# Performance work log

Hardware: AMD Instinct MI355X
Metric: run time of the kernel (lower is better)

## Reference

```python
import jax, jax.numpy as jnp
import numpy as np

D_MODEL = 1024
N_HEADS = 16
HEAD_DIM = D_MODEL // N_HEADS
D_FF = 4 * D_MODEL
LN_EPS = 1e-5


def setup_inputs() -> dict:
    key = jax.random.key(0)
    ks = jax.random.split(key, 12)
    B, T = 16, 512
    s = lambda fan_in: 1.0 / np.sqrt(fan_in)
    inp = {
        'x': jax.random.normal(ks[0], (B, T, D_MODEL), jnp.float32),
        # torch Linear layout: [out_features, in_features]
        'w_qkv': jax.random.normal(ks[1], (3 * D_MODEL, D_MODEL), jnp.float32) * s(D_MODEL),
        'w_proj': jax.random.normal(ks[2], (D_MODEL, D_MODEL), jnp.float32) * s(D_MODEL),
        'w_ff1': jax.random.normal(ks[3], (D_FF, D_MODEL), jnp.float32) * s(D_MODEL),
        'b_ff1': jax.random.normal(ks[4], (D_FF,), jnp.float32) * 0.02,
        'w_ff2': jax.random.normal(ks[5], (D_MODEL, D_FF), jnp.float32) * s(D_FF),
        'b_ff2': jax.random.normal(ks[6], (D_MODEL,), jnp.float32) * 0.02,
        'ln1_g': jnp.ones((D_MODEL,), jnp.float32),
        'ln1_b': jnp.zeros((D_MODEL,), jnp.float32),
        'ln2_g': jnp.ones((D_MODEL,), jnp.float32),
        'ln2_b': jnp.zeros((D_MODEL,), jnp.float32),
    }
    return inp


def _layernorm(x, g, b):
    mu = jnp.mean(x, axis=-1, keepdims=True)
    var = jnp.var(x, axis=-1, keepdims=True)
    return (x - mu) * jax.lax.rsqrt(var + LN_EPS) * g + b


def _block(x, w_qkv, w_proj, w_ff1, b_ff1, w_ff2, b_ff2, ln1_g, ln1_b, ln2_g, ln2_b):
    B, T, _ = x.shape
    a = _layernorm(x, ln1_g, ln1_b)
    qkv = a @ w_qkv.T  # [B,T,3D]
    q, k, v = jnp.split(qkv, 3, axis=-1)
    # [B,H,T,hd]
    rs = lambda t: t.reshape(B, T, N_HEADS, HEAD_DIM).transpose(0, 2, 1, 3)
    q, k, v = rs(q), rs(k), rs(v)
    scale = HEAD_DIM ** -0.5
    att = jnp.einsum('bhqd,bhkd->bhqk', q, k) * scale
    causal = jnp.tril(jnp.ones((T, T), bool))
    att = jnp.where(causal, att, jnp.float32(-10000.0))
    att = jax.nn.softmax(att, axis=-1)
    out = jnp.einsum('bhqk,bhkd->bhqd', att, v)
    out = out.transpose(0, 2, 1, 3).reshape(B, T, D_MODEL)
    x = x + out @ w_proj.T
    f = _layernorm(x, ln2_g, ln2_b)
    f = jax.nn.gelu(f @ w_ff1.T + b_ff1, approximate=False) @ w_ff2.T + b_ff2
    return x + f


def reference(x, w_qkv, w_proj, w_ff1, b_ff1, w_ff2, b_ff2, ln1_g, ln1_b, ln2_g, ln2_b):
    return _block(x, w_qkv, w_proj, w_ff1, b_ff1, w_ff2, b_ff2, ln1_g, ln1_b, ln2_g, ln2_b)
```

## Files before the change

kernel.cpp:

```cpp
#include <hip/hip_runtime.h>
#include <stdint.h>

typedef __bf16 bf16x8_t __attribute__((ext_vector_type(8)));
typedef float f32x4_t __attribute__((ext_vector_type(4)));
typedef unsigned short ushort8_t __attribute__((ext_vector_type(8)));

#define DEV __device__ __forceinline__

DEV unsigned short f2bf(float f) {
  union { float f; uint32_t u; } v; v.f = f;
  uint32_t r = v.u + 0x7FFFu + ((v.u >> 16) & 1u);
  return (unsigned short)(r >> 16);
}

DEV void gl_lds16(const void* g, void* l) {
  __builtin_amdgcn_global_load_lds(
      (const __attribute__((address_space(1))) void*)g,
      (__attribute__((address_space(3))) void*)l, 16, 0, 0);
}

DEV float gelu_f(float x) {
  const float y = x * 0.7071067811865475f;
  const float ay = fabsf(y);
  const float t = __builtin_amdgcn_rcpf(1.0f + 0.3275911f * ay);
  float p = fmaf(t, 1.061405429f, -1.453152027f);
  p = fmaf(t, p, 1.421413741f);
  p = fmaf(t, p, -0.284496736f);
  p = fmaf(t, p, 0.254829592f);
  p *= t;
  const float e = __expf(-ay * ay);
  float erfv = 1.0f - p * e;
  erfv = copysignf(erfv, y);
  return 0.5f * x * (1.0f + erfv);
}

__global__ __launch_bounds__(256) void cvt_all(const float* __restrict__ w0, unsigned short* __restrict__ o0,
                                               const float* __restrict__ w1, unsigned short* __restrict__ o1,
                                               const float* __restrict__ w2, unsigned short* __restrict__ o2,
                                               const float* __restrict__ w3, unsigned short* __restrict__ o3) {
  int i = blockIdx.x * 256 + threadIdx.x;
  const float* in; unsigned short* outp;
  if (i < 786432) { in = w0; outp = o0; }
  else if (i < 1048576) { in = w1; outp = o1; i -= 786432; }
  else if (i < 2097152) { in = w2; outp = o2; i -= 1048576; }
  else { in = w3; outp = o3; i -= 2097152; }
  float4 v = ((const float4*)in)[i];
  ushort4 o;
  o.x = f2bf(v.x); o.y = f2bf(v.y); o.z = f2bf(v.z); o.w = f2bf(v.w);
  ((ushort4*)outp)[i] = o;
}

__global__ __launch_bounds__(256) void ln_kernel(const float* __restrict__ x,
                                                 const float* __restrict__ g,
                                                 const float* __restrict__ b,
                                                 unsigned short* __restrict__ outp) {
  const int row = blockIdx.x * 4 + (threadIdx.x >> 6);
  const int lane = threadIdx.x & 63;
  const float4* xr = (const float4*)(x + (size_t)row * 1024);
  float4 v[4];
  float s = 0.f, s2 = 0.f;
#pragma unroll
  for (int j = 0; j < 4; ++j) {
    v[j] = xr[j * 64 + lane];
    s += v[j].x + v[j].y + v[j].z + v[j].w;
    s2 += v[j].x * v[j].x + v[j].y * v[j].y + v[j].z * v[j].z + v[j].w * v[j].w;
  }
#pragma unroll
  for (int off = 1; off < 64; off <<= 1) {
    s += __shfl_xor(s, off, 64);
    s2 += __shfl_xor(s2, off, 64);
  }
  const float mu = s * (1.0f / 1024.0f);
  const float var = s2 * (1.0f / 1024.0f) - mu * mu;
  const float rstd = rsqrtf(var + 1e-5f);
  ushort4* orow = (ushort4*)(outp + (size_t)row * 1024);
  const float4* gp = (const float4*)g;
  const float4* bp = (const float4*)b;
#pragma unroll
  for (int j = 0; j < 4; ++j) {
    float4 gv = gp[j * 64 + lane], bv = bp[j * 64 + lane];
    ushort4 o;
    o.x = f2bf((v[j].x - mu) * rstd * gv.x + bv.x);
    o.y = f2bf((v[j].y - mu) * rstd * gv.y + bv.y);
    o.z = f2bf((v[j].z - mu) * rstd * gv.z + bv.z);
    o.w = f2bf((v[j].w - mu) * rstd * gv.w + bv.w);
    orow[j * 64 + lane] = o;
  }
}

template <int MODE, int BM>
__global__ __launch_bounds__(256) void gemm_bt(const unsigned short* __restrict__ A,
                                               const unsigned short* __restrict__ B,
                                               float* __restrict__ Cf,
                                               unsigned short* __restrict__ Cb,
                                               const float* __restrict__ bias,
                                               const float* __restrict__ res,
                                               unsigned short* __restrict__ Vt,
                                               int M, int N, int K) {
  constexpr int MI = BM / 32;
  constexpr int RT = 8192 / BM;
  constexpr int ABUF = BM * 32;
  __shared__ unsigned short sA[2][ABUF];
  __shared__ unsigned short sB[2][128 * 32];
  const int tid = threadIdx.x;
  const int w = tid >> 6, lane = tid & 63;
  const int kg = lane >> 4, l16 = lane & 15;
  const int wm = (w & 1) * (BM / 2), wn = (w >> 1) * 64;

  const int cid = blockIdx.y * gridDim.x + blockIdx.x;
  const int colBase = (cid / RT) * 128;
  const int rowBase = (cid % RT) * BM;

  const int sr = (BM == 128) ? (tid >> 2) : ((tid >> 2) & 63);
  const int gc = ((tid & 3) ^ ((sr >> 1) & 3)) * 8;
  const unsigned short* gA = A + (size_t)(rowBase + sr) * K + gc;
  const unsigned short* gB = B + (size_t)(colBase + sr) * K + gc;

  f32x4_t acc[MI][4];
#pragma unroll
  for (int mi = 0; mi < MI; ++mi)
#pragma unroll
    for (int ni = 0; ni < 4; ++ni) acc[mi][ni] = (f32x4_t)0.0f;

  int offA[MI], offB[4];
  const int pc = (kg ^ ((l16 >> 1) & 3)) * 8;
#pragma unroll
  for (int i = 0; i < MI; ++i) offA[i] = (wm + i * 16 + l16) * 32 + pc;
#pragma unroll
  for (int i = 0; i < 4; ++i) offB[i] = (wn + i * 16 + l16) * 32 + pc;

  gl_lds16(gA, &sA[0][tid * 8]);
  if (BM == 128) gl_lds16(gA + (size_t)64 * K, &sA[0][2048 + tid * 8]);
  gl_lds16(gB, &sB[0][tid * 8]);
  gl_lds16(gB + (size_t)64 * K, &sB[0][2048 + tid * 8]);
  gA += 32; gB += 32;

  const int nk = K >> 5;
  for (int kt = 0; kt < nk; ++kt) {
    __syncthreads();
    if (kt + 1 < nk) {
      const int nb = (kt + 1) & 1;
      gl_lds16(gA, &sA[nb][tid * 8]);
      if (BM == 128) gl_lds16(gA + (size_t)64 * K, &sA[nb][2048 + tid * 8]);
      gl_lds16(gB, &sB[nb][tid * 8]);
      gl_lds16(gB + (size_t)64 * K, &sB[nb][2048 + tid * 8]);
      gA += 32; gB += 32;
    }
    const int par = kt & 1;
    bf16x8_t a[MI], b[4];
#pragma unroll
    for (int i = 0; i < MI; ++i) a[i] = *(const bf16x8_t*)(&sA[par][0] + offA[i]);
#pragma unroll
    for (int i = 0; i < 4; ++i) b[i] = *(const bf16x8_t*)(&sB[par][0] + offB[i]);
#pragma unroll
    for (int mi = 0; mi < MI; ++mi)
#pragma unroll
      for (int ni = 0; ni < 4; ++ni)
        acc[mi][ni] = __builtin_amdgcn_mfma_f32_16x16x32_bf16(a[mi], b[ni], acc[mi][ni], 0, 0, 0);
  }

#pragma unroll
  for (int mi = 0; mi < MI; ++mi) {
#pragma unroll
    for (int ni = 0; ni < 4; ++ni) {
      const int col = colBase + wn + ni * 16 + l16;
      if (MODE == 0 && colBase >= 2048) {
        const int c2 = col - 2048;
        const int hh = c2 >> 6, dd = c2 & 63;
        const int rw = rowBase + wm + mi * 16 + kg * 4;
        ushort4 pk;
        pk.x = f2bf(acc[mi][ni][0]);
        pk.y = f2bf(acc[mi][ni][1]);
        pk.z = f2bf(acc[mi][ni][2]);
        pk.w = f2bf(acc[mi][ni][3]);
        *(ushort4*)(Vt + (((size_t)(rw >> 9) * 16 + hh) * 64 + dd) * 512 + (rw & 511)) = pk;
        continue;
      }
      float bv = 0.f;
      if (MODE == 2 || MODE == 3) bv = bias[col];
#pragma unroll
      for (int r = 0; r < 4; ++r) {
        const int row = rowBase + wm + mi * 16 + kg * 4 + r;
        const size_t idx = (size_t)row * N + col;
        float v = acc[mi][ni][r];
        if (MODE == 0) {
          Cb[idx] = f2bf(v);
        } else if (MODE == 1) {
          Cf[idx] = v + res[idx];
        } else if (MODE == 2) {
          Cb[idx] = f2bf(gelu_f(v + bv));
        } else {
          Cf[idx] = v + bv + res[idx];
        }
      }
    }
  }
}

__global__ __launch_bounds__(256) void attn_kernel(const unsigned short* __restrict__ qkv,
                                                   const unsigned short* __restrict__ Vt,
                                                   unsigned short* __restrict__ outp) {
  constexpr int D3 = 3072;
  __shared__ unsigned short sQ[128 * 64];
  __shared__ unsigned short sK[64 * 64];
  __shared__ unsigned short sVt[64 * 64];
  __shared__ unsigned short sP[128 * 72];
  const int tid = threadIdx.x;
  const int w = tid >> 6, lane = tid & 63;
  const int kg = lane >> 4, l16 = lane & 15;
  const int qi = (int)gridDim.x - 1 - (int)blockIdx.x;
  const int h = blockIdx.y, bb = blockIdx.z;
  const int t0 = qi * 128;
  const size_t base = (size_t)bb * 512 * D3 + h * 64;

  const int sr = tid >> 3;
  const int sc = ((tid & 7) ^ (sr & 7)) * 8;

  {
    const unsigned short* g = qkv + base + (size_t)(t0 + sr) * D3 + sc;
    unsigned short* l = sQ + tid * 8;
#pragma unroll
    for (int i = 0; i < 4; ++i) gl_lds16(g + (size_t)32 * i * D3, l + 2048 * i);
  }

  const unsigned short* gVbase = Vt + ((size_t)(bb * 16 + h) * 64 + sr) * 512 + sc;

  bf16x8_t ones;
#pragma unroll
  for (int j = 0; j < 8; ++j) ones[j] = (__bf16)1.0f;

  const int wm = w * 32;
  f32x4_t o[2][4];
  f32x4_t lsum[2];
#pragma unroll
  for (int mi = 0; mi < 2; ++mi) {
    lsum[mi] = (f32x4_t)0.0f;
#pragma unroll
    for (int di = 0; di < 4; ++di) o[mi][di] = (f32x4_t)0.0f;
  }

  const int nkt = (qi + 1) * 2;
  for (int kt = 0; kt < nkt; ++kt) {
    const int k0 = kt * 64;
    __syncthreads();
    {
      const unsigned short* g = qkv + base + 1024 + (size_t)(k0 + sr) * D3 + sc;
      unsigned short* l = sK + tid * 8;
      gl_lds16(g, l);
      gl_lds16(g + (size_t)32 * D3, l + 2048);
    }
    {
      const unsigned short* g = gVbase + k0;
      unsigned short* l = sVt + tid * 8;
      gl_lds16(g, l);
      gl_lds16(g + (size_t)32 * 512, l + 2048);
    }
    __syncthreads();

    const bool active = (k0 <= t0 + wm + 31);
    if (active) {
      f32x4_t s[2][4];
#pragma unroll
      for (int mi = 0; mi < 2; ++mi)
#pragma unroll
        for (int ni = 0; ni < 4; ++ni) s[mi][ni] = (f32x4_t)0.0f;
#pragma unroll
      for (int kd = 0; kd < 2; ++kd) {
        bf16x8_t aq[2], bk[4];
#pragma unroll
        for (int mi = 0; mi < 2; ++mi) {
          const int rr = wm + mi * 16 + l16;
          aq[mi] = *(const bf16x8_t*)(sQ + rr * 64 + (((kd * 4 + kg) ^ (l16 & 7)) * 8));
        }
#pragma unroll
        for (int ni = 0; ni < 4; ++ni) {
          const int rr = ni * 16 + l16;
          bk[ni] = *(const bf16x8_t*)(sK + rr * 64 + (((kd * 4 + kg) ^ (l16 & 7)) * 8));
        }
#pragma unroll
        for (int mi = 0; mi < 2; ++mi)
#pragma unroll
          for (int ni = 0; ni < 4; ++ni)
            s[mi][ni] = __builtin_amdgcn_mfma_f32_16x16x32_bf16(aq[mi], bk[ni], s[mi][ni], 0, 0, 0);
      }
#pragma unroll
      for (int mi = 0; mi < 2; ++mi) {
#pragma unroll
        for (int r = 0; r < 4; ++r) {
          const int q = t0 + wm + mi * 16 + kg * 4 + r;
          const int prow = wm + mi * 16 + kg * 4 + r;
#pragma unroll
          for (int ni = 0; ni < 4; ++ni) {
            const int kk = k0 + ni * 16 + l16;
            const float p = (kk <= q) ? __expf(s[mi][ni][r] * 0.125f) : 0.0f;
            sP[prow * 72 + ni * 16 + l16] = f2bf(p);
          }
        }
      }
#pragma unroll
      for (int kd = 0; kd < 2; ++kd) {
        bf16x8_t ap[2], bv[4];
#pragma unroll
        for (int mi = 0; mi < 2; ++mi)
          ap[mi] = *(const bf16x8_t*)(sP + (wm + mi * 16 + l16) * 72 + kd * 32 + kg * 8);
#pragma unroll
        for (int di = 0; di < 4; ++di) {
          const int dd = di * 16 + l16;
          bv[di] = *(const bf16x8_t*)(sVt + dd * 64 + (((kd * 4 + kg) ^ (l16 & 7)) * 8));
        }
#pragma unroll
        for (int mi = 0; mi < 2; ++mi) {
#pragma unroll
          for (int di = 0; di < 4; ++di)
            o[mi][di] = __builtin_amdgcn_mfma_f32_16x16x32_bf16(ap[mi], bv[di], o[mi][di], 0, 0, 0);
          lsum[mi] = __builtin_amdgcn_mfma_f32_16x16x32_bf16(ap[mi], ones, lsum[mi], 0, 0, 0);
        }
      }
    }
  }

#pragma unroll
  for (int mi = 0; mi < 2; ++mi) {
#pragma unroll
    for (int r = 0; r < 4; ++r) {
      const float inv = 1.0f / lsum[mi][r];
      const int row = t0 + wm + mi * 16 + kg * 4 + r;
      const size_t ob = ((size_t)bb * 512 + row) * 1024 + h * 64;
#pragma unroll
      for (int di = 0; di < 4; ++di)
        outp[ob + di * 16 + l16] = f2bf(o[mi][di][r] * inv);
    }
  }
}

extern "C" void kernel_launch(void* const* d_in, const int* in_sizes, int n_in,
                              void* d_out, int out_size, void* d_ws, size_t ws_size,
                              hipStream_t stream) {
  const float* x      = (const float*)d_in[0];
  const float* w_qkv  = (const float*)d_in[1];
  const float* w_proj = (const float*)d_in[2];
  const float* w_ff1  = (const float*)d_in[3];
  const float* b_ff1  = (const float*)d_in[4];
  const float* w_ff2  = (const float*)d_in[5];
  const float* b_ff2  = (const float*)d_in[6];
  const float* ln1_g  = (const float*)d_in[7];
  const float* ln1_b  = (const float*)d_in[8];
  const float* ln2_g  = (const float*)d_in[9];
  const float* ln2_b  = (const float*)d_in[10];
  float* out = (float*)d_out;
  char* ws = (char*)d_ws;

  unsigned short* wqkv_b  = (unsigned short*)(ws + 0);
  unsigned short* wproj_b = (unsigned short*)(ws + 6291456);
  unsigned short* wff1_b  = (unsigned short*)(ws + 8388608);
  unsigned short* wff2_b  = (unsigned short*)(ws + 16777216);
  unsigned short* a_b     = (unsigned short*)(ws + 25165824);
  float*          x2_f    = (float*)(ws + 41943040);
  unsigned short* vt_b    = (unsigned short*)(ws + 41943040);
  unsigned short* qkv_b   = (unsigned short*)(ws + 75497472);
  unsigned short* attn_b  = (unsigned short*)(ws + 125829120);
  unsigned short* h_b     = qkv_b;

  cvt_all<<<12288, 256, 0, stream>>>(w_qkv, wqkv_b, w_proj, wproj_b, w_ff1, wff1_b, w_ff2, wff2_b);

  ln_kernel<<<2048, 256, 0, stream>>>(x, ln1_g, ln1_b, a_b);
  gemm_bt<0, 128><<<dim3(24, 64), 256, 0, stream>>>(a_b, wqkv_b, nullptr, qkv_b, nullptr, nullptr, vt_b, 8192, 3072, 1024);
  attn_kernel<<<dim3(4, 16, 16), 256, 0, stream>>>(qkv_b, vt_b, attn_b);
  gemm_bt<1, 64><<<dim3(8, 128), 256, 0, stream>>>(attn_b, wproj_b, x2_f, nullptr, nullptr, x, nullptr, 8192, 1024, 1024);
  ln_kernel<<<2048, 256, 0, stream>>>(x2_f, ln2_g, ln2_b, a_b);
  gemm_bt<2, 128><<<dim3(32, 64), 256, 0, stream>>>(a_b, wff1_b, nullptr, h_b, b_ff1, nullptr, nullptr, 8192, 4096, 1024);
  gemm_bt<3, 64><<<dim3(8, 128), 256, 0, stream>>>(h_b, wff2_b, out, nullptr, b_ff2, x2_f, nullptr, 8192, 1024, 4096);
}
```

Baseline: 475.0 us.

## Replace GEMM with 256x256 tile, 8-wave pipelined kernel using interleaved loads and MFMA

Replaces the 128x128/64x128 double-buffered GEMM with a 512-thread kernel that computes 256x256 output tiles over K-steps of 64. Global-to-LDS loads are split into quarters and interleaved with four MFMA phases, with raised wave priority around the MFMA bursts and explicit barriers and waitcnts. Workgroup IDs are remapped for XCD locality. The intent is more reuse per tile and better overlap of memory with matrix work. The cost is that the N=1024 GEMMs launch only 128 workgroups, which may underfill the GPU, and the hand-placed waitcnt and barrier scheme is fragile.

```diff
diff --git a/kernel.cpp b/kernel.cpp
--- a/kernel.cpp
+++ b/kernel.cpp
@@ -3,7 +3,6 @@
 
 typedef __bf16 bf16x8_t __attribute__((ext_vector_type(8)));
 typedef float f32x4_t __attribute__((ext_vector_type(4)));
-typedef unsigned short ushort8_t __attribute__((ext_vector_type(8)));
 
 #define DEV __device__ __forceinline__
 
@@ -17,6 +16,12 @@
   __builtin_amdgcn_global_load_lds(
       (const __attribute__((address_space(1))) void*)g,
       (__attribute__((address_space(3))) void*)l, 16, 0, 0);
+}
+
+DEV void barx() {
+  asm volatile("" ::: "memory");
+  __builtin_amdgcn_s_barrier();
+  asm volatile("" ::: "memory");
 }
 
 DEV float gelu_f(float x) {
@@ -88,79 +93,120 @@
   }
 }
 
-template <int MODE, int BM>
-__global__ __launch_bounds__(256) void gemm_bt(const unsigned short* __restrict__ A,
-                                               const unsigned short* __restrict__ B,
-                                               float* __restrict__ Cf,
-                                               unsigned short* __restrict__ Cb,
-                                               const float* __restrict__ bias,
-                                               const float* __restrict__ res,
-                                               unsigned short* __restrict__ Vt,
-                                               int M, int N, int K) {
-  constexpr int MI = BM / 32;
-  constexpr int RT = 8192 / BM;
-  constexpr int ABUF = BM * 32;
-  __shared__ unsigned short sA[2][ABUF];
-  __shared__ unsigned short sB[2][128 * 32];
+
+#define RD_A(MH, PC)                                                        \
+  _Pragma("unroll") for (int mi = 0; mi < 4; ++mi)                          \
+      a[mi] = *(const bf16x8_t*)(pA + (wm + (MH)*64 + mi * 16 + l16) * 64 + (PC));
+
+#define RD_B(DST, PC)                                                       \
+  _Pragma("unroll") for (int ni = 0; ni < 4; ++ni)                          \
+      DST[ni] = *(const bf16x8_t*)(pB + (wn + ni * 16 + l16) * 64 + (PC));
+
+#define MFMA16(MH, BB)                                                      \
+  __builtin_amdgcn_s_setprio(1);                                            \
+  _Pragma("unroll") for (int mi = 0; mi < 4; ++mi)                          \
+  _Pragma("unroll") for (int ni = 0; ni < 4; ++ni)                          \
+      acc[(MH)*4 + mi][ni] = __builtin_amdgcn_mfma_f32_16x16x32_bf16(       \
+          a[mi], BB[ni], acc[(MH)*4 + mi][ni], 0, 0, 0);                    \
+  __builtin_amdgcn_s_setprio(0);
+
+template <int MODE>
+__global__ __launch_bounds__(512) void gemm8(const unsigned short* __restrict__ A,
+                                             const unsigned short* __restrict__ B,
+                                             float* __restrict__ Cf,
+                                             unsigned short* __restrict__ Cb,
+                                             const float* __restrict__ bias,
+                                             const float* __restrict__ res,
+                                             unsigned short* __restrict__ Vt,
+                                             int M, int N, int K) {
+  __shared__ unsigned short sA[2][256 * 64];
+  __shared__ unsigned short sB[2][256 * 64];
   const int tid = threadIdx.x;
   const int w = tid >> 6, lane = tid & 63;
   const int kg = lane >> 4, l16 = lane & 15;
-  const int wm = (w & 1) * (BM / 2), wn = (w >> 1) * 64;
-
-  const int cid = blockIdx.y * gridDim.x + blockIdx.x;
-  const int colBase = (cid / RT) * 128;
-  const int rowBase = (cid % RT) * BM;
-
-  const int sr = (BM == 128) ? (tid >> 2) : ((tid >> 2) & 63);
-  const int gc = ((tid & 3) ^ ((sr >> 1) & 3)) * 8;
-  const unsigned short* gA = A + (size_t)(rowBase + sr) * K + gc;
-  const unsigned short* gB = B + (size_t)(colBase + sr) * K + gc;
-
-  f32x4_t acc[MI][4];
-#pragma unroll
-  for (int mi = 0; mi < MI; ++mi)
+  const int wm = (w & 1) * 128, wn = (w >> 1) * 64;
+
+  const int nwg = gridDim.x;
+  const int bid = blockIdx.x;
+  const int cid = (bid & 7) * (nwg >> 3) + (bid >> 3);
+  const int rowBase = (cid & 31) * 256;
+  const int colBase = (cid >> 5) * 256;
+
+  const int srow = tid >> 3, sch = tid & 7;
+  const unsigned short* aBase = A + (size_t)(rowBase + srow) * K + ((sch ^ (srow & 7)) * 8);
+  const unsigned short* bBase = B + (size_t)(colBase + srow) * K + ((sch ^ (srow & 7)) * 8);
+  const int sdo = tid * 8;
+
+  f32x4_t acc[8][4];
+#pragma unroll
+  for (int mi = 0; mi < 8; ++mi)
 #pragma unroll
     for (int ni = 0; ni < 4; ++ni) acc[mi][ni] = (f32x4_t)0.0f;
 
-  int offA[MI], offB[4];
-  const int pc = (kg ^ ((l16 >> 1) & 3)) * 8;
-#pragma unroll
-  for (int i = 0; i < MI; ++i) offA[i] = (wm + i * 16 + l16) * 32 + pc;
-#pragma unroll
-  for (int i = 0; i < 4; ++i) offB[i] = (wn + i * 16 + l16) * 32 + pc;
-
-  gl_lds16(gA, &sA[0][tid * 8]);
-  if (BM == 128) gl_lds16(gA + (size_t)64 * K, &sA[0][2048 + tid * 8]);
-  gl_lds16(gB, &sB[0][tid * 8]);
-  gl_lds16(gB + (size_t)64 * K, &sB[0][2048 + tid * 8]);
-  gA += 32; gB += 32;
-
-  const int nk = K >> 5;
-  for (int kt = 0; kt < nk; ++kt) {
-    __syncthreads();
-    if (kt + 1 < nk) {
-      const int nb = (kt + 1) & 1;
-      gl_lds16(gA, &sA[nb][tid * 8]);
-      if (BM == 128) gl_lds16(gA + (size_t)64 * K, &sA[nb][2048 + tid * 8]);
-      gl_lds16(gB, &sB[nb][tid * 8]);
-      gl_lds16(gB + (size_t)64 * K, &sB[nb][2048 + tid * 8]);
-      gA += 32; gB += 32;
-    }
-    const int par = kt & 1;
-    bf16x8_t a[MI], b[4];
-#pragma unroll
-    for (int i = 0; i < MI; ++i) a[i] = *(const bf16x8_t*)(&sA[par][0] + offA[i]);
-#pragma unroll
-    for (int i = 0; i < 4; ++i) b[i] = *(const bf16x8_t*)(&sB[par][0] + offB[i]);
-#pragma unroll
-    for (int mi = 0; mi < MI; ++mi)
-#pragma unroll
-      for (int ni = 0; ni < 4; ++ni)
-        acc[mi][ni] = __builtin_amdgcn_mfma_f32_16x16x32_bf16(a[mi], b[ni], acc[mi][ni], 0, 0, 0);
-  }
-
-#pragma unroll
-  for (int mi = 0; mi < MI; ++mi) {
+  const int nt = K >> 6;
+  const int pc0 = ((kg ^ (l16 & 7)) & 7) * 8;
+  const int pc1 = (((4 + kg) ^ (l16 & 7)) & 7) * 8;
+
+#pragma unroll
+  for (int R = 0; R < 4; ++R)
+    gl_lds16(aBase + (size_t)(R * 64) * K, &sA[0][R * 4096 + sdo]);
+#pragma unroll
+  for (int Cq = 0; Cq < 4; ++Cq)
+    gl_lds16(bBase + (size_t)(Cq * 64) * K, &sB[0][Cq * 4096 + sdo]);
+  {
+    const size_t k1 = (nt > 1) ? 64 : 0;
+    gl_lds16(aBase + k1, &sA[1][sdo]);
+    gl_lds16(aBase + (size_t)128 * K + k1, &sA[1][8192 + sdo]);
+  }
+  asm volatile("s_waitcnt vmcnt(2)" ::: "memory");
+  barx();
+
+  for (int kt = 0; kt < nt; ++kt) {
+    const int cur = kt & 1;
+    const unsigned short* pA = &sA[cur][0];
+    const unsigned short* pB = &sB[cur][0];
+    unsigned short* nAd = &sA[cur ^ 1][0];
+    unsigned short* nBd = &sB[cur ^ 1][0];
+    unsigned short* pAd = &sA[cur][0];
+    const size_t kA1 = (size_t)((kt + 1 < nt) ? (kt + 1) : (nt - 1)) * 64;
+    const size_t kA2 = (size_t)((kt + 2 < nt) ? (kt + 2) : 0) * 64;
+
+    bf16x8_t a[4], b0[4], b1[4];
+
+    RD_A(0, pc0)
+    RD_B(b0, pc0)
+    gl_lds16(aBase + (size_t)64 * K + kA1, nAd + 4096 + sdo);
+    gl_lds16(aBase + (size_t)192 * K + kA1, nAd + 12288 + sdo);
+    barx();
+    MFMA16(0, b0)
+    barx();
+
+    RD_A(0, pc1)
+    RD_B(b1, pc1)
+    gl_lds16(bBase + kA1, nBd + sdo);
+    gl_lds16(bBase + (size_t)64 * K + kA1, nBd + 4096 + sdo);
+    barx();
+    MFMA16(0, b1)
+    barx();
+
+    RD_A(1, pc0)
+    gl_lds16(bBase + (size_t)128 * K + kA1, nBd + 8192 + sdo);
+    gl_lds16(bBase + (size_t)192 * K + kA1, nBd + 12288 + sdo);
+    barx();
+    MFMA16(1, b0)
+    barx();
+
+    RD_A(1, pc1)
+    gl_lds16(aBase + kA2, pAd + sdo);
+    gl_lds16(aBase + (size_t)128 * K + kA2, pAd + 8192 + sdo);
+    barx();
+    MFMA16(1, b1)
+    asm volatile("s_waitcnt vmcnt(2)" ::: "memory");
+    barx();
+  }
+
+#pragma unroll
+  for (int mi = 0; mi < 8; ++mi) {
 #pragma unroll
     for (int ni = 0; ni < 4; ++ni) {
       const int col = colBase + wn + ni * 16 + l16;
@@ -195,6 +241,7 @@
       }
     }
   }
+  asm volatile("s_waitcnt vmcnt(0)" ::: "memory");
 }
 
 __global__ __launch_bounds__(256) void attn_kernel(const unsigned short* __restrict__ qkv,
@@ -364,10 +411,10 @@
   cvt_all<<<12288, 256, 0, stream>>>(w_qkv, wqkv_b, w_proj, wproj_b, w_ff1, wff1_b, w_ff2, wff2_b);
 
   ln_kernel<<<2048, 256, 0, stream>>>(x, ln1_g, ln1_b, a_b);
-  gemm_bt<0, 128><<<dim3(24, 64), 256, 0, stream>>>(a_b, wqkv_b, nullptr, qkv_b, nullptr, nullptr, vt_b, 8192, 3072, 1024);
+  gemm8<0><<<384, 512, 0, stream>>>(a_b, wqkv_b, nullptr, qkv_b, nullptr, nullptr, vt_b, 8192, 3072, 1024);
   attn_kernel<<<dim3(4, 16, 16), 256, 0, stream>>>(qkv_b, vt_b, attn_b);
-  gemm_bt<1, 64><<<dim3(8, 128), 256, 0, stream>>>(attn_b, wproj_b, x2_f, nullptr, nullptr, x, nullptr, 8192, 1024, 1024);
+  gemm8<1><<<128, 512, 0, stream>>>(attn_b, wproj_b, x2_f, nullptr, nullptr, x, nullptr, 8192, 1024, 1024);
   ln_kernel<<<2048, 256, 0, stream>>>(x2_f, ln2_g, ln2_b, a_b);
-  gemm_bt<2, 128><<<dim3(32, 64), 256, 0, stream>>>(a_b, wff1_b, nullptr, h_b, b_ff1, nullptr, nullptr, 8192, 4096, 1024);
-  gemm_bt<3, 64><<<dim3(8, 128), 256, 0, stream>>>(h_b, wff2_b, out, nullptr, b_ff2, x2_f, nullptr, 8192, 1024, 4096);
-}
+  gemm8<2><<<512, 512, 0, stream>>>(a_b, wff1_b, nullptr, h_b, b_ff1, nullptr, nullptr, 8192, 4096, 1024);
+  gemm8<3><<<128, 512, 0, stream>>>(h_b, wff2_b, out, nullptr, b_ff2, x2_f, nullptr, 8192, 1024, 4096);
+}
```

Measured after the change: 530.6 us. 1.12x slower.
